# Kernel optimization log

Hardware: AMD Instinct MI355X
Metric: run time of the kernel (lower is better)

The kernel has to match this reference:

```python
import jax, jax.numpy as jnp
import numpy as np
from jax import lax

B, N, C_IN = 16, 4096, 64
RATIO, R, K = 0.25, 0.2, 32
MLP = [64, 64, 128]
EPS = 1e-5  # BatchNorm eps


def setup_inputs() -> dict:
    key = jax.random.key(0)
    ks = jax.random.split(key, 8)
    inp = {
        "x": jax.random.normal(ks[0], (B, N, C_IN), jnp.float32),
        "pos": jax.random.uniform(ks[1], (B, N, 3), jnp.float32),
    }
    dims = [C_IN + 3] + MLP  # [67, 64, 64, 128]
    for i in range(3):
        scale = float(np.sqrt(2.0 / dims[i]))
        inp[f"W{i+1}"] = jax.random.normal(ks[2 + i], (dims[i], dims[i + 1]), jnp.float32) * scale
        inp[f"g{i+1}"] = jnp.ones((dims[i + 1],), jnp.float32)   # BN gamma
        inp[f"b{i+1}"] = jnp.zeros((dims[i + 1],), jnp.float32)  # BN beta
        inp[f"rm{i+1}"] = jnp.zeros((dims[i + 1],), jnp.float32) # BN running mean
        inp[f"rv{i+1}"] = jnp.ones((dims[i + 1],), jnp.float32)  # BN running var
    return inp


def _fps(pos, m):
    """Farthest point sampling on one cloud pos [N,3]; deterministic start at 0."""
    n = pos.shape[0]

    def body(i, carry):
        mind, idxs = carry
        last = pos[idxs[i - 1]]
        mind = jnp.minimum(mind, jnp.sum((pos - last) ** 2, axis=-1))
        idxs = idxs.at[i].set(jnp.argmax(mind).astype(jnp.int32))
        return mind, idxs

    mind0 = jnp.full((n,), 1e10, pos.dtype)
    idxs0 = jnp.zeros((m,), jnp.int32)
    _, idxs = lax.fori_loop(1, m, body, (mind0, idxs0))
    return idxs


def reference(x, pos, W1, g1, b1, rm1, rv1, W2, g2, b2, rm2, rv2, W3, g3, b3, rm3, rv3):
    bb, n, _ = pos.shape
    m = int(round(n * RATIO))
    # ---- FPS (indices are constants wrt grads) ----
    idx = jax.vmap(lambda p: _fps(p, m))(lax.stop_gradient(pos))        # [B,M]
    cpos = jnp.take_along_axis(pos, idx[..., None], axis=1)             # [B,M,3]
    # ---- ball query: first K points (in index order) within radius R ----
    d2 = jnp.sum((cpos[:, :, None, :] - pos[:, None, :, :]) ** 2, -1)   # [B,M,N]
    score = jnp.where(d2 <= R * R, n - jnp.arange(n, dtype=jnp.int32), 0)
    topv = lax.top_k(score, K)[0]                                       # [B,M,K]
    valid = topv > 0  # centroid itself is always within radius -> >=1 valid
    nidx = jnp.where(valid, n - topv, 0)                                # [B,M,K]
    # ---- gather neighbors + relative positions ----
    flat = nidx.reshape(bb, m * K)
    x_j = jnp.take_along_axis(x, flat[..., None], axis=1).reshape(bb, m, K, -1)
    pos_j = jnp.take_along_axis(pos, flat[..., None], axis=1).reshape(bb, m, K, 3)
    h = jnp.concatenate([x_j, pos_j - cpos[:, :, None, :]], axis=-1)    # [B,M,K,67]
    # ---- shared MLP: Linear(no bias) -> BN(eval) -> ReLU, x3 ----
    for (W, g, b, rm, rv) in ((W1, g1, b1, rm1, rv1), (W2, g2, b2, rm2, rv2), (W3, g3, b3, rm3, rv3)):
        h = jax.nn.relu((h @ W - rm) * (g * lax.rsqrt(rv + EPS)) + b)
    # ---- scatter-max aggregation over neighbors ----
    h = jnp.where(valid[..., None], h, -jnp.inf)
    x_out = jnp.max(h, axis=2)                                          # [B,M,128]
    return x_out, cpos
```

## Files before the change

### kernel.cpp

```cpp
#include <hip/hip_runtime.h>
#include <hip/hip_bf16.h>
#include <float.h>
#include <math.h>

#define BATCH 16
#define NPTS  4096
#define CIN   64
#define MCENT 1024
#define KNB   32
#define OUT_X (BATCH * MCENT * 128)

__device__ __forceinline__ float f_sub(float a, float b){ float r; asm("v_sub_f32 %0, %1, %2" : "=v"(r) : "v"(a), "v"(b)); return r; }
__device__ __forceinline__ float f_mul(float a, float b){ float r; asm("v_mul_f32 %0, %1, %2" : "=v"(r) : "v"(a), "v"(b)); return r; }
__device__ __forceinline__ float f_add(float a, float b){ float r; asm("v_add_f32 %0, %1, %2" : "=v"(r) : "v"(a), "v"(b)); return r; }

__device__ __forceinline__ float dist2_exact(float px, float py, float pz,
                                             float lx, float ly, float lz) {
    float dx = f_sub(px, lx), dy = f_sub(py, ly), dz = f_sub(pz, lz);
    return f_add(f_add(f_mul(dx, dx), f_mul(dy, dy)), f_mul(dz, dz));
}

template <int CTRL>
__device__ __forceinline__ float dpp_max(float x) {
    int xi = __float_as_int(x);
    int yi = __builtin_amdgcn_update_dpp(xi, xi, CTRL, 0xF, 0xF, false);
    return fmaxf(x, __int_as_float(yi));
}
__device__ __forceinline__ float wave_max_f32(float v) {
    v = dpp_max<0xB1>(v);
    v = dpp_max<0x4E>(v);
    v = dpp_max<0x141>(v);
    v = dpp_max<0x140>(v);
    int s = __builtin_amdgcn_ds_swizzle(__float_as_int(v), 0x401F);
    v = fmaxf(v, __int_as_float(s));
    float a = v, b = v;
    asm("v_permlane32_swap_b32 %0, %1" : "+v"(a), "+v"(b));
    return fmaxf(a, b);
}

__global__ __launch_bounds__(512, 1) void fps_kernel(
    const float* __restrict__ pos, float* __restrict__ cpos)
{
    __shared__ float spx[NPTS], spy[NPTS], spz[NPTS];
    __shared__ unsigned long long slot[4];
    __shared__ int widxarr[MCENT];

    const int b = blockIdx.x;
    const int t = threadIdx.x;
    const float* pb = pos + (size_t)b * NPTS * 3;

    float px[8], py[8], pz[8], mind[8];
    {
        const float4* src = (const float4*)(pb + t * 24);
        float v[24];
#pragma unroll
        for (int q = 0; q < 6; ++q) {
            float4 f = src[q];
            v[q * 4 + 0] = f.x; v[q * 4 + 1] = f.y; v[q * 4 + 2] = f.z; v[q * 4 + 3] = f.w;
        }
#pragma unroll
        for (int j = 0; j < 8; ++j) {
            int n = t * 8 + j;
            px[j] = v[j * 3 + 0]; py[j] = v[j * 3 + 1]; pz[j] = v[j * 3 + 2];
            spx[n] = px[j]; spy[n] = py[j]; spz[n] = pz[j];
            mind[j] = 1e10f;
        }
    }
    if (t == 0) {
        slot[0] = 0ull; slot[1] = 0ull; slot[2] = 0ull; slot[3] = 0ull;
        widxarr[0] = 0;
    }
    __syncthreads();

    int w = 0;
    for (int i = 1; i < MCENT; ++i) {
        float lx = spx[w], ly = spy[w], lz = spz[w];
#pragma unroll
        for (int j = 0; j < 8; ++j) {
            float d = dist2_exact(px[j], py[j], pz[j], lx, ly, lz);
            mind[j] = fminf(mind[j], d);
        }
        float tmax = fmaxf(fmaxf(fmaxf(mind[0], mind[1]), fmaxf(mind[2], mind[3])),
                           fmaxf(fmaxf(mind[4], mind[5]), fmaxf(mind[6], mind[7])));
        float wmax = wave_max_f32(tmax);
        if (tmax == wmax) {
            int cand = 0;
#pragma unroll
            for (int j = 7; j >= 0; --j)
                if (mind[j] == wmax) cand = t * 8 + j;
            unsigned long long key =
                ((unsigned long long)__float_as_uint(wmax) << 32) |
                (unsigned)(NPTS - 1 - cand);
            atomicMax(&slot[i & 3], key);
        }
        if (t == 0) slot[(i + 2) & 3] = 0ull;
        __syncthreads();
        unsigned long long win = slot[i & 3];
        w = (NPTS - 1) - (int)(unsigned)(win & 0xFFFFFFFFull);
        if (t == 0) widxarr[i] = w;
    }
    __syncthreads();
#pragma unroll
    for (int e = 0; e < 2; ++e) {
        int c = t + e * 512;
        int src = widxarr[c];
        float* cp = cpos + ((size_t)b * MCENT + c) * 3;
        cp[0] = spx[src]; cp[1] = spy[src]; cp[2] = spz[src];
    }
}

__global__ __launch_bounds__(256) void ballq_kernel(
    const float* __restrict__ pos, const float* __restrict__ cpos,
    int* __restrict__ nidx)
{
    const int wid  = blockIdx.x * 4 + (threadIdx.x >> 6);
    const int lane = threadIdx.x & 63;
    const int b    = wid >> 10;
    const float* pb = pos + (size_t)b * NPTS * 3;
    const float cx = cpos[wid * 3 + 0];
    const float cy = cpos[wid * 3 + 1];
    const float cz = cpos[wid * 3 + 2];
    const float R2 = (float)(0.2 * 0.2);
    int* outp = nidx + (size_t)wid * KNB;

    int cnt = 0;
    for (int j0 = 0; j0 < NPTS; j0 += 64) {
        int j = j0 + lane;
        float x = pb[j * 3 + 0], y = pb[j * 3 + 1], z = pb[j * 3 + 2];
        float d = dist2_exact(x, y, z, cx, cy, cz);
        bool valid = (d <= R2);
        unsigned long long msk = __ballot(valid);
        if (valid) {
            int rank = cnt + __popcll(msk & ((1ull << lane) - 1ull));
            if (rank < KNB) outp[rank] = j;
        }
        cnt += __popcll(msk);
        if (cnt >= KNB) break;
    }
    int nv = cnt < KNB ? cnt : KNB;
    if (lane >= nv && lane < KNB) outp[lane] = -1;
}

__global__ __launch_bounds__(256, 1) void mlp_kernel(
    const float* __restrict__ x, const float* __restrict__ pos,
    const float* __restrict__ W1, const float* __restrict__ g1, const float* __restrict__ b1,
    const float* __restrict__ rm1, const float* __restrict__ rv1,
    const float* __restrict__ W2, const float* __restrict__ g2, const float* __restrict__ b2,
    const float* __restrict__ rm2, const float* __restrict__ rv2,
    const float* __restrict__ W3, const float* __restrict__ g3, const float* __restrict__ b3,
    const float* __restrict__ rm3, const float* __restrict__ rv3,
    const float* __restrict__ cpos, const int* __restrict__ nidx,
    float* __restrict__ out)
{
    __shared__ float hbuf[256 * 69];
    __shared__ float sscale[256], sbias[256];

    const int t   = threadIdx.x;
    const int g   = t >> 5;
    const int k   = t & 31;
    const int cid0 = blockIdx.x * 8;
    const int cid  = cid0 + g;
    const int b    = cid >> 10;

    {
        float gg, bb, rm, rv;
        if (t < 64)       { gg = g1[t];     bb = b1[t];     rm = rm1[t];     rv = rv1[t]; }
        else if (t < 128) { int c = t - 64;  gg = g2[c]; bb = b2[c]; rm = rm2[c]; rv = rv2[c]; }
        else              { int c = t - 128; gg = g3[c]; bb = b3[c]; rm = rm3[c]; rv = rv3[c]; }
        float s = gg / sqrtf(rv + 1e-5f);
        sscale[t] = s;
        sbias[t]  = bb - rm * s;
    }

    const int j = nidx[(size_t)cid * KNB + k];
    const bool valid = (j >= 0);
    float* hrow = &hbuf[t * 69];
    if (valid) {
        const float* xr = x + ((size_t)b * NPTS + j) * CIN;
#pragma unroll
        for (int q = 0; q < 16; ++q) {
            float4 v = ((const float4*)xr)[q];
            hrow[q * 4 + 0] = v.x; hrow[q * 4 + 1] = v.y;
            hrow[q * 4 + 2] = v.z; hrow[q * 4 + 3] = v.w;
        }
        const float* pr = pos + ((size_t)b * NPTS + j) * 3;
        hrow[64] = f_sub(pr[0], cpos[cid * 3 + 0]);
        hrow[65] = f_sub(pr[1], cpos[cid * 3 + 1]);
        hrow[66] = f_sub(pr[2], cpos[cid * 3 + 2]);
    } else {
        for (int q = 0; q < 67; ++q) hrow[q] = 0.f;
    }
    __syncthreads();

    float acc[64];
#pragma unroll
    for (int c = 0; c < 64; ++c) acc[c] = 0.f;
#pragma unroll 2
    for (int kk = 0; kk < 67; ++kk) {
        float hv = hrow[kk];
        const float* wr = W1 + kk * 64;
#pragma unroll
        for (int c = 0; c < 64; ++c) acc[c] = fmaf(hv, wr[c], acc[c]);
    }
#pragma unroll
    for (int c = 0; c < 64; ++c)
        hrow[c] = fmaxf(fmaf(acc[c], sscale[c], sbias[c]), 0.f);

#pragma unroll
    for (int c = 0; c < 64; ++c) acc[c] = 0.f;
#pragma unroll 2
    for (int kk = 0; kk < 64; ++kk) {
        float hv = hrow[kk];
        const float* wr = W2 + kk * 64;
#pragma unroll
        for (int c = 0; c < 64; ++c) acc[c] = fmaf(hv, wr[c], acc[c]);
    }
#pragma unroll
    for (int c = 0; c < 64; ++c)
        hrow[c] = fmaxf(fmaf(acc[c], sscale[64 + c], sbias[64 + c]), 0.f);

    float acc3[128];
#pragma unroll
    for (int c = 0; c < 128; ++c) acc3[c] = 0.f;
#pragma unroll 2
    for (int kk = 0; kk < 64; ++kk) {
        float hv = hrow[kk];
        const float* wr = W3 + kk * 128;
#pragma unroll
        for (int c = 0; c < 128; ++c) acc3[c] = fmaf(hv, wr[c], acc3[c]);
    }
#pragma unroll
    for (int c = 0; c < 128; ++c) {
        float v = fmaxf(fmaf(acc3[c], sscale[128 + c], sbias[128 + c]), 0.f);
        acc3[c] = valid ? v : -FLT_MAX;
    }

#pragma unroll
    for (int half = 0; half < 2; ++half) {
        __syncthreads();
#pragma unroll
        for (int c = 0; c < 64; ++c) hbuf[t * 69 + c] = acc3[half * 64 + c];
        __syncthreads();
#pragma unroll
        for (int e0 = 0; e0 < 2; ++e0) {
            int e  = t + e0 * 256;
            int gg = e >> 6, c = e & 63;
            float mv = -FLT_MAX;
#pragma unroll
            for (int kk2 = 0; kk2 < 32; ++kk2)
                mv = fmaxf(mv, hbuf[(gg * 32 + kk2) * 69 + c]);
            out[((size_t)(cid0 + gg)) * 128 + half * 64 + c] = mv;
        }
    }
}

extern "C" void kernel_launch(void* const* d_in, const int* in_sizes, int n_in,
                              void* d_out, int out_size, void* d_ws, size_t ws_size,
                              hipStream_t stream) {
    const float* x   = (const float*)d_in[0];
    const float* pos = (const float*)d_in[1];
    const float* W1  = (const float*)d_in[2];
    const float* g1  = (const float*)d_in[3];
    const float* b1  = (const float*)d_in[4];
    const float* rm1 = (const float*)d_in[5];
    const float* rv1 = (const float*)d_in[6];
    const float* W2  = (const float*)d_in[7];
    const float* g2  = (const float*)d_in[8];
    const float* b2  = (const float*)d_in[9];
    const float* rm2 = (const float*)d_in[10];
    const float* rv2 = (const float*)d_in[11];
    const float* W3  = (const float*)d_in[12];
    const float* g3  = (const float*)d_in[13];
    const float* b3  = (const float*)d_in[14];
    const float* rm3 = (const float*)d_in[15];
    const float* rv3 = (const float*)d_in[16];

    float* out  = (float*)d_out;
    float* cpos = out + OUT_X;
    int*   nidx = (int*)d_ws;

    fps_kernel<<<dim3(BATCH), dim3(512), 0, stream>>>(pos, cpos);
    ballq_kernel<<<dim3(BATCH * MCENT / 4), dim3(256), 0, stream>>>(pos, cpos, nidx);
    mlp_kernel<<<dim3(BATCH * MCENT / 8), dim3(256), 0, stream>>>(
        x, pos, W1, g1, b1, rm1, rv1, W2, g2, b2, rm2, rv2,
        W3, g3, b3, rm3, rv3, cpos, nidx, out);
}
```

Before: 1.120 ms.

## Replace FPS shared atomics with per-wave keys; keep MLP rows in registers

FPS now picks each wave's argmax with a ballot and shuffle, writes one key per wave to a double-buffered shared array, and every thread reduces the eight keys after one barrier. This replaces the shared 64-bit atomicMax and the slot reset, and the point coordinates move into a float4 shared array so one load fetches the last centroid. In the MLP kernel the per-neighbor feature row stays in registers instead of shared memory, the layer loops are fully unrolled, and the max over neighbors uses cross-lane DPP and swizzle reductions instead of a shared-memory transpose behind two barriers. Register pressure in the MLP kernel rises sharply, with 67+64+128 floats live, so spilling is a risk.

```diff
diff --git a/kernel.cpp b/kernel.cpp
--- a/kernel.cpp
+++ b/kernel.cpp
@@ -26,13 +26,16 @@
     int yi = __builtin_amdgcn_update_dpp(xi, xi, CTRL, 0xF, 0xF, false);
     return fmaxf(x, __int_as_float(yi));
 }
-__device__ __forceinline__ float wave_max_f32(float v) {
+__device__ __forceinline__ float half_max_f32(float v) {
     v = dpp_max<0xB1>(v);
     v = dpp_max<0x4E>(v);
     v = dpp_max<0x141>(v);
     v = dpp_max<0x140>(v);
     int s = __builtin_amdgcn_ds_swizzle(__float_as_int(v), 0x401F);
-    v = fmaxf(v, __int_as_float(s));
+    return fmaxf(v, __int_as_float(s));
+}
+__device__ __forceinline__ float wave_max_f32(float v) {
+    v = half_max_f32(v);
     float a = v, b = v;
     asm("v_permlane32_swap_b32 %0, %1" : "+v"(a), "+v"(b));
     return fmaxf(a, b);
@@ -41,12 +44,13 @@
 __global__ __launch_bounds__(512, 1) void fps_kernel(
     const float* __restrict__ pos, float* __restrict__ cpos)
 {
-    __shared__ float spx[NPTS], spy[NPTS], spz[NPTS];
-    __shared__ unsigned long long slot[4];
+    __shared__ __align__(16) float4 sp[NPTS];
+    __shared__ __align__(16) unsigned long long swkey[2][8];
     __shared__ int widxarr[MCENT];
 
     const int b = blockIdx.x;
     const int t = threadIdx.x;
+    const int lane = t & 63, wv = t >> 6;
     const float* pb = pos + (size_t)b * NPTS * 3;
 
     float px[8], py[8], pz[8], mind[8];
@@ -56,56 +60,57 @@
 #pragma unroll
         for (int q = 0; q < 6; ++q) {
             float4 f = src[q];
-            v[q * 4 + 0] = f.x; v[q * 4 + 1] = f.y; v[q * 4 + 2] = f.z; v[q * 4 + 3] = f.w;
-        }
-#pragma unroll
-        for (int j = 0; j < 8; ++j) {
-            int n = t * 8 + j;
-            px[j] = v[j * 3 + 0]; py[j] = v[j * 3 + 1]; pz[j] = v[j * 3 + 2];
-            spx[n] = px[j]; spy[n] = py[j]; spz[n] = pz[j];
-            mind[j] = 1e10f;
-        }
-    }
-    if (t == 0) {
-        slot[0] = 0ull; slot[1] = 0ull; slot[2] = 0ull; slot[3] = 0ull;
-        widxarr[0] = 0;
-    }
+            v[q*4+0]=f.x; v[q*4+1]=f.y; v[q*4+2]=f.z; v[q*4+3]=f.w;
+        }
+#pragma unroll
+        for (int jj = 0; jj < 8; ++jj) {
+            int n = t * 8 + jj;
+            px[jj]=v[jj*3+0]; py[jj]=v[jj*3+1]; pz[jj]=v[jj*3+2];
+            sp[n] = make_float4(px[jj], py[jj], pz[jj], 0.f);
+            mind[jj] = 1e10f;
+        }
+    }
+    if (t == 0) widxarr[0] = 0;
     __syncthreads();
 
     int w = 0;
     for (int i = 1; i < MCENT; ++i) {
-        float lx = spx[w], ly = spy[w], lz = spz[w];
-#pragma unroll
-        for (int j = 0; j < 8; ++j) {
-            float d = dist2_exact(px[j], py[j], pz[j], lx, ly, lz);
-            mind[j] = fminf(mind[j], d);
-        }
-        float tmax = fmaxf(fmaxf(fmaxf(mind[0], mind[1]), fmaxf(mind[2], mind[3])),
-                           fmaxf(fmaxf(mind[4], mind[5]), fmaxf(mind[6], mind[7])));
+        float4 L = sp[w];
+#pragma unroll
+        for (int jj = 0; jj < 8; ++jj) {
+            float d = dist2_exact(px[jj], py[jj], pz[jj], L.x, L.y, L.z);
+            mind[jj] = fminf(mind[jj], d);
+        }
+        float tmax = fmaxf(fmaxf(fmaxf(mind[0],mind[1]), fmaxf(mind[2],mind[3])),
+                           fmaxf(fmaxf(mind[4],mind[5]), fmaxf(mind[6],mind[7])));
         float wmax = wave_max_f32(tmax);
-        if (tmax == wmax) {
-            int cand = 0;
-#pragma unroll
-            for (int j = 7; j >= 0; --j)
-                if (mind[j] == wmax) cand = t * 8 + j;
-            unsigned long long key =
-                ((unsigned long long)__float_as_uint(wmax) << 32) |
-                (unsigned)(NPTS - 1 - cand);
-            atomicMax(&slot[i & 3], key);
-        }
-        if (t == 0) slot[(i + 2) & 3] = 0ull;
+        int cand = 0;
+#pragma unroll
+        for (int jj = 7; jj >= 0; --jj)
+            if (mind[jj] == wmax) cand = t * 8 + jj;
+        unsigned long long msk = __ballot(tmax == wmax);
+        int first = __ffsll(msk) - 1;
+        int candw = __shfl(cand, first);
+        if (lane == 0)
+            swkey[i & 1][wv] = ((unsigned long long)__float_as_uint(wmax) << 32)
+                             | (unsigned)(NPTS - 1 - candw);
         __syncthreads();
-        unsigned long long win = slot[i & 3];
-        w = (NPTS - 1) - (int)(unsigned)(win & 0xFFFFFFFFull);
+        unsigned long long best = swkey[i & 1][0];
+#pragma unroll
+        for (int q = 1; q < 8; ++q) {
+            unsigned long long o = swkey[i & 1][q];
+            best = o > best ? o : best;
+        }
+        w = (NPTS - 1) - (int)(unsigned)(best & 0xFFFFFFFFull);
         if (t == 0) widxarr[i] = w;
     }
     __syncthreads();
 #pragma unroll
     for (int e = 0; e < 2; ++e) {
         int c = t + e * 512;
-        int src = widxarr[c];
+        float4 P = sp[widxarr[c]];
         float* cp = cpos + ((size_t)b * MCENT + c) * 3;
-        cp[0] = spx[src]; cp[1] = spy[src]; cp[2] = spz[src];
+        cp[0] = P.x; cp[1] = P.y; cp[2] = P.z;
     }
 }
 
@@ -152,8 +157,8 @@
     const float* __restrict__ cpos, const int* __restrict__ nidx,
     float* __restrict__ out)
 {
-    __shared__ float hbuf[256 * 69];
-    __shared__ float sscale[256], sbias[256];
+    __shared__ __align__(16) float sscale[256];
+    __shared__ __align__(16) float sbias[256];
 
     const int t   = threadIdx.x;
     const int g   = t >> 5;
@@ -174,82 +179,96 @@
 
     const int j = nidx[(size_t)cid * KNB + k];
     const bool valid = (j >= 0);
-    float* hrow = &hbuf[t * 69];
+    float h[67];
     if (valid) {
-        const float* xr = x + ((size_t)b * NPTS + j) * CIN;
+        const float4* xr = (const float4*)(x + ((size_t)b * NPTS + j) * CIN);
 #pragma unroll
         for (int q = 0; q < 16; ++q) {
-            float4 v = ((const float4*)xr)[q];
-            hrow[q * 4 + 0] = v.x; hrow[q * 4 + 1] = v.y;
-            hrow[q * 4 + 2] = v.z; hrow[q * 4 + 3] = v.w;
+            float4 v = xr[q];
+            h[q*4+0]=v.x; h[q*4+1]=v.y; h[q*4+2]=v.z; h[q*4+3]=v.w;
         }
         const float* pr = pos + ((size_t)b * NPTS + j) * 3;
-        hrow[64] = f_sub(pr[0], cpos[cid * 3 + 0]);
-        hrow[65] = f_sub(pr[1], cpos[cid * 3 + 1]);
-        hrow[66] = f_sub(pr[2], cpos[cid * 3 + 2]);
+        h[64] = f_sub(pr[0], cpos[cid * 3 + 0]);
+        h[65] = f_sub(pr[1], cpos[cid * 3 + 1]);
+        h[66] = f_sub(pr[2], cpos[cid * 3 + 2]);
     } else {
-        for (int q = 0; q < 67; ++q) hrow[q] = 0.f;
+#pragma unroll
+        for (int q = 0; q < 67; ++q) h[q] = 0.f;
     }
     __syncthreads();
 
     float acc[64];
 #pragma unroll
     for (int c = 0; c < 64; ++c) acc[c] = 0.f;
-#pragma unroll 2
+#pragma unroll
     for (int kk = 0; kk < 67; ++kk) {
-        float hv = hrow[kk];
+        const float hv = h[kk];
         const float* wr = W1 + kk * 64;
 #pragma unroll
         for (int c = 0; c < 64; ++c) acc[c] = fmaf(hv, wr[c], acc[c]);
     }
 #pragma unroll
-    for (int c = 0; c < 64; ++c)
-        hrow[c] = fmaxf(fmaf(acc[c], sscale[c], sbias[c]), 0.f);
+    for (int c4 = 0; c4 < 16; ++c4) {
+        float4 sc = *(const float4*)&sscale[c4 * 4];
+        float4 sb = *(const float4*)&sbias[c4 * 4];
+        h[c4*4+0] = fmaxf(fmaf(acc[c4*4+0], sc.x, sb.x), 0.f);
+        h[c4*4+1] = fmaxf(fmaf(acc[c4*4+1], sc.y, sb.y), 0.f);
+        h[c4*4+2] = fmaxf(fmaf(acc[c4*4+2], sc.z, sb.z), 0.f);
+        h[c4*4+3] = fmaxf(fmaf(acc[c4*4+3], sc.w, sb.w), 0.f);
+    }
 
 #pragma unroll
     for (int c = 0; c < 64; ++c) acc[c] = 0.f;
-#pragma unroll 2
+#pragma unroll
     for (int kk = 0; kk < 64; ++kk) {
-        float hv = hrow[kk];
+        const float hv = h[kk];
         const float* wr = W2 + kk * 64;
 #pragma unroll
         for (int c = 0; c < 64; ++c) acc[c] = fmaf(hv, wr[c], acc[c]);
     }
 #pragma unroll
-    for (int c = 0; c < 64; ++c)
-        hrow[c] = fmaxf(fmaf(acc[c], sscale[64 + c], sbias[64 + c]), 0.f);
+    for (int c4 = 0; c4 < 16; ++c4) {
+        float4 sc = *(const float4*)&sscale[64 + c4 * 4];
+        float4 sb = *(const float4*)&sbias[64 + c4 * 4];
+        h[c4*4+0] = fmaxf(fmaf(acc[c4*4+0], sc.x, sb.x), 0.f);
+        h[c4*4+1] = fmaxf(fmaf(acc[c4*4+1], sc.y, sb.y), 0.f);
+        h[c4*4+2] = fmaxf(fmaf(acc[c4*4+2], sc.z, sb.z), 0.f);
+        h[c4*4+3] = fmaxf(fmaf(acc[c4*4+3], sc.w, sb.w), 0.f);
+    }
 
     float acc3[128];
 #pragma unroll
     for (int c = 0; c < 128; ++c) acc3[c] = 0.f;
-#pragma unroll 2
+#pragma unroll
     for (int kk = 0; kk < 64; ++kk) {
-        float hv = hrow[kk];
+        const float hv = h[kk];
         const float* wr = W3 + kk * 128;
 #pragma unroll
         for (int c = 0; c < 128; ++c) acc3[c] = fmaf(hv, wr[c], acc3[c]);
     }
 #pragma unroll
-    for (int c = 0; c < 128; ++c) {
-        float v = fmaxf(fmaf(acc3[c], sscale[128 + c], sbias[128 + c]), 0.f);
-        acc3[c] = valid ? v : -FLT_MAX;
-    }
-
-#pragma unroll
-    for (int half = 0; half < 2; ++half) {
-        __syncthreads();
-#pragma unroll
-        for (int c = 0; c < 64; ++c) hbuf[t * 69 + c] = acc3[half * 64 + c];
-        __syncthreads();
-#pragma unroll
-        for (int e0 = 0; e0 < 2; ++e0) {
-            int e  = t + e0 * 256;
-            int gg = e >> 6, c = e & 63;
-            float mv = -FLT_MAX;
-#pragma unroll
-            for (int kk2 = 0; kk2 < 32; ++kk2)
-                mv = fmaxf(mv, hbuf[(gg * 32 + kk2) * 69 + c]);
-            out[((size_t)(cid0 + gg)) * 128 + half * 64 + c] = mv;
+    for (int c4 = 0; c4 < 32; ++c4) {
+        float4 sc = *(const float4*)&sscale[128 + c4 * 4];
+        float4 sb = *(const float4*)&sbias[128 + c4 * 4];
+        acc3[c4*4+0] = fmaxf(fmaf(acc3[c4*4+0], sc.x, sb.x), 0.f);
+        acc3[c4*4+1] = fmaxf(fmaf(acc3[c4*4+1], sc.y, sb.y), 0.f);
+        acc3[c4*4+2] = fmaxf(fmaf(acc3[c4*4+2], sc.z, sb.z), 0.f);
+        acc3[c4*4+3] = fmaxf(fmaf(acc3[c4*4+3], sc.w, sb.w), 0.f);
+    }
+    if (!valid) {
+#pragma unroll
+        for (int c = 0; c < 128; ++c) acc3[c] = -FLT_MAX;
+    }
+
+#pragma unroll
+    for (int c = 0; c < 128; ++c) acc3[c] = half_max_f32(acc3[c]);
+
+    if (k == 0) {
+        float* op = out + (size_t)cid * 128;
+#pragma unroll
+        for (int c4 = 0; c4 < 32; ++c4) {
+            *(float4*)(op + c4 * 4) =
+                make_float4(acc3[c4*4+0], acc3[c4*4+1], acc3[c4*4+2], acc3[c4*4+3]);
         }
     }
 }
```

Measured after the change: 3.049 ms. 2.72x slower.
